# Kernel tuning notes

Measured on AMD Instinct MI355X. Metric: run time of the kernel, lower is better.

Reference implementation:

```python
import jax, jax.numpy as jnp
import numpy as np

P = 3; Q = 3                 # spline degrees (deg_p, deg_q)
OUT_U = 64; OUT_V = 64       # surface evaluation grid
W_CTRL = 1.0; W_SURF = 1.0
B = 1024; MU_MAX = 32; MV_MAX = 32
EPS = 1e-5                   # SurfEval samples u,v in [eps, 1-eps]


def _open_uniform_knots(n_valid, degree, n_max):
    """Clamped open-uniform knot vector for n_valid ctrl pts, padded to static
    length n_max+degree+1. Entries beyond the valid span are clamped to 1.0,
    which makes the padded basis functions identically zero on [eps, 1-eps]."""
    L = n_valid + degree + 1  # true (ragged) knot count, traced int
    k = jnp.arange(n_max + degree + 1)
    interior = k.astype(jnp.float32) / (L - 1).astype(jnp.float32)
    return jnp.where(k <= degree, 0.0, jnp.where(k >= L - 1 - degree, 1.0, interior))


def _bspline_basis(kv, degree, u):
    """Cox-de Boor, vectorized over u. kv: (n_max+degree+1,), u: (U,).
    Returns (U, n_max) basis matrix; padded columns are exactly zero."""
    N = ((u[None, :] >= kv[:-1, None]) & (u[None, :] < kv[1:, None])).astype(jnp.float32)
    for d in range(1, degree + 1):
        m = N.shape[0] - 1  # number of basis funcs at this level
        den1 = kv[d:d + m] - kv[:m]
        den2 = kv[d + 1:d + 1 + m] - kv[1:1 + m]
        s1 = jnp.where((den1 > 0)[:, None],
                       (u[None, :] - kv[:m, None]) / jnp.where(den1 > 0, den1, 1.0)[:, None], 0.0)
        s2 = jnp.where((den2 > 0)[:, None],
                       (kv[d + 1:d + 1 + m, None] - u[None, :]) / jnp.where(den2 > 0, den2, 1.0)[:, None], 0.0)
        N = s1 * N[:m] + s2 * N[1:m + 1]
    return N.T  # (U, n_max)


def _eval_surface(ctrl, mask_b, u, v):
    """NURBS surface eval for one sample with ragged (Mu_i, Mv_i) via padded
    knots/basis; unit weights => rational division by basis partition sum."""
    mu = jnp.maximum(jnp.sum(jnp.any(mask_b > 0, axis=1)), P + 1)
    mv = jnp.maximum(jnp.sum(jnp.any(mask_b > 0, axis=0)), Q + 1)
    Bu = _bspline_basis(_open_uniform_knots(mu, P, MU_MAX), P, u)  # (OUT_U, MU_MAX)
    Bv = _bspline_basis(_open_uniform_knots(mv, Q, MV_MAX), Q, v)  # (OUT_V, MV_MAX)
    num = jnp.einsum('ui,vj,ijd->uvd', Bu, Bv, ctrl)               # (OUT_U, OUT_V, 3)
    den = Bu.sum(-1)[:, None] * Bv.sum(-1)[None, :]                # unit-weight denom
    return num / den[..., None]


def setup_inputs() -> dict:
    key = jax.random.key(0)
    k1, k2, k3, k4, k5 = jax.random.split(key, 5)
    # ragged true control sizes per sample, >= degree+1
    mu = jax.random.randint(k1, (B,), P + 1, MU_MAX + 1)
    mv = jax.random.randint(k2, (B,), Q + 1, MV_MAX + 1)
    mask = ((jnp.arange(MU_MAX)[None, :, None] < mu[:, None, None]) &
            (jnp.arange(MV_MAX)[None, None, :] < mv[:, None, None])).astype(jnp.float32)
    ctrl_pred_pad = jax.random.normal(k3, (B, MU_MAX, MV_MAX, 3), jnp.float32)
    ctrl_gt_pad = jax.random.normal(k4, (B, MU_MAX, MV_MAX, 3), jnp.float32)
    xyz_samples = jax.random.normal(k5, (B, OUT_U, OUT_V, 3), jnp.float32)
    return {"ctrl_pred_pad": ctrl_pred_pad, "ctrl_gt_pad": ctrl_gt_pad,
            "mask": mask, "xyz_samples": xyz_samples}


def reference(ctrl_pred_pad, ctrl_gt_pad, mask, xyz_samples):
    # masked control-point MSE
    diff2 = ((ctrl_pred_pad - ctrl_gt_pad) ** 2).sum(-1)
    loss_ctrl = (diff2 * mask).sum() / jnp.maximum(mask.sum() * 3.0, 1.0)
    # batched ragged surface evaluation
    u = jnp.linspace(EPS, 1.0 - EPS, OUT_U)
    v = jnp.linspace(EPS, 1.0 - EPS, OUT_V)
    surf = jax.vmap(lambda c, m: _eval_surface(c, m, u, v))(ctrl_pred_pad, mask)
    loss_surf = jnp.mean((surf.reshape(B, -1, 3) - xyz_samples.reshape(B, -1, 3)) ** 2)
    total = W_CTRL * loss_ctrl + W_SURF * loss_surf  # original computes total BEFORE nan-guard
    bad = jnp.isnan(surf).any() | jnp.isinf(surf).any()
    surf_mse = jnp.where(bad, jnp.float32(1e6), loss_surf)
    return total, loss_ctrl, surf_mse
```

## Files before the change

### kernel.cpp

```cpp
#include <hip/hip_runtime.h>
#include <math.h>

#define MU_MAXC 32
#define MV_MAXC 32
#define OUT_UC  64
#define OUT_VC  64
#define DEG     3
#define NKNOT   (MU_MAXC + DEG + 1)
#define EPSV    1e-5f

__global__ void zero_ws_kernel(double* acc, int* bad) {
    acc[0] = 0.0; acc[1] = 0.0; acc[2] = 0.0; bad[0] = 0;
}

template <int MODE>
__launch_bounds__(256, 5)
__global__ void nurbs_loss_kernel(const float* __restrict__ ctrl_pred,
                                  const float* __restrict__ ctrl_gt,
                                  const float* __restrict__ mask,
                                  const float* __restrict__ xyz,
                                  double* __restrict__ pd, int Bcnt,
                                  int* __restrict__ badp)
{
    const int b   = blockIdx.x;
    const int tid = threadIdx.x;

    __shared__ float s_tmp[OUT_UC * MV_MAXC * 3];
    __shared__ float s_Bu4[4 * OUT_UC];
    __shared__ float s_Bv4[4 * OUT_VC];
    __shared__ int   s_uoff[OUT_UC];
    __shared__ int   s_voff[OUT_VC];
    __shared__ float s_sumBu[OUT_UC];
    __shared__ float s_sumBv[OUT_VC];
    __shared__ float s_knots_u[NKNOT];
    __shared__ float s_knots_v[NKNOT];
    __shared__ int   s_rowany[MU_MAXC];
    __shared__ int   s_colany[MV_MAXC];
    __shared__ int   s_mu, s_mv, s_bad;
    __shared__ float s_wred[4], s_wred2[4];
    __shared__ float s_ctrl_diff, s_ctrl_mask;

    if (tid < 32) { s_rowany[tid] = 0; s_colany[tid] = 0; }
    if (tid == 0) s_bad = 0;
    __syncthreads();

    float lsum_mask = 0.f, lsum_diff = 0.f;
    for (int k = 0; k < 4; k++) {
        const int cell = tid + 256 * k;
        const int base = (b * 1024 + cell) * 3;
        const float m  = mask[b * 1024 + cell];
        const float p0 = ctrl_pred[base + 0], p1 = ctrl_pred[base + 1], p2 = ctrl_pred[base + 2];
        const float g0 = ctrl_gt[base + 0],   g1 = ctrl_gt[base + 1],   g2 = ctrl_gt[base + 2];
        const float d0 = p0 - g0, d1 = p1 - g1, d2 = p2 - g2;
        lsum_mask += m;
        lsum_diff += m * (d0 * d0 + d1 * d1 + d2 * d2);
        if (m > 0.f) { s_rowany[cell >> 5] = 1; s_colany[cell & 31] = 1; }
    }
    #pragma unroll
    for (int off = 32; off > 0; off >>= 1) {
        lsum_mask += __shfl_down(lsum_mask, off);
        lsum_diff += __shfl_down(lsum_diff, off);
    }
    if ((tid & 63) == 0) { s_wred[tid >> 6] = lsum_mask; s_wred2[tid >> 6] = lsum_diff; }
    __syncthreads();

    if (tid == 0) {
        int cu = 0, cv = 0;
        #pragma unroll
        for (int i = 0; i < 32; i++) { cu += s_rowany[i]; cv += s_colany[i]; }
        s_mu = cu > (DEG + 1) ? cu : (DEG + 1);
        s_mv = cv > (DEG + 1) ? cv : (DEG + 1);
        s_ctrl_mask = s_wred[0] + s_wred[1] + s_wred[2] + s_wred[3];
        s_ctrl_diff = s_wred2[0] + s_wred2[1] + s_wred2[2] + s_wred2[3];
    }
    __syncthreads();

    if (tid < NKNOT) {
        const int L = s_mu + DEG + 1;
        s_knots_u[tid] = (tid <= DEG) ? 0.f
                        : ((tid >= L - 1 - DEG) ? 1.f : (float)tid / (float)(L - 1));
    } else if (tid >= 64 && tid < 64 + NKNOT) {
        const int k = tid - 64;
        const int L = s_mv + DEG + 1;
        s_knots_v[k] = (k <= DEG) ? 0.f
                      : ((k >= L - 1 - DEG) ? 1.f : (float)k / (float)(L - 1));
    }
    __syncthreads();

    if (tid < 128) {
        const bool isU = tid < 64;
        const int t = isU ? tid : (tid - 64);
        const float* kv = isU ? s_knots_u : s_knots_v;
        const float step = (1.f - 2.f * EPSV) / 63.f;
        const float uu = (t == 63) ? (1.f - EPSV) : (EPSV + step * (float)t);

        int span = DEG;
        #pragma unroll
        for (int k = DEG + 1; k < NKNOT - 1; k++)
            if (kv[k] <= uu) span = k;

        float N4[DEG + 1], left[DEG + 1], right[DEG + 1];
        N4[0] = 1.f;
        #pragma unroll
        for (int j = 1; j <= DEG; j++) {
            left[j]  = uu - kv[span + 1 - j];
            right[j] = kv[span + j] - uu;
            float saved = 0.f;
            #pragma unroll
            for (int r = 0; r < j; r++) {
                const float temp = N4[r] / (right[r + 1] + left[j - r]);
                N4[r] = saved + right[r + 1] * temp;
                saved = left[j - r] * temp;
            }
            N4[j] = saved;
        }
        const float s = N4[0] + N4[1] + N4[2] + N4[3];
        const int off = span - DEG;
        if (isU) {
            #pragma unroll
            for (int r = 0; r < 4; r++) s_Bu4[r * 64 + t] = N4[r];
            s_uoff[t] = off; s_sumBu[t] = s;
        } else {
            #pragma unroll
            for (int r = 0; r < 4; r++) s_Bv4[r * 64 + t] = N4[r];
            s_voff[t] = off; s_sumBv[t] = s;
        }
    }
    __syncthreads();

    const float* ctrlb = ctrl_pred + (size_t)b * 1024 * 3;
    for (int k = 0; k < 24; k++) {
        const int flat = tid + 256 * k;
        const int u = flat / 96;
        const int jd = flat - u * 96;
        const int off = s_uoff[u];
        float a = 0.f;
        #pragma unroll
        for (int r = 0; r < 4; r++)
            a += s_Bu4[r * 64 + u] * ctrlb[(off + r) * 96 + jd];
        s_tmp[flat] = a;
    }
    __syncthreads();

    float lsum_surf = 0.f;
    int bad = 0;
    for (int k = 0; k < 16; k++) {
        const int p = tid + 256 * k;
        const int u = p >> 6, v = p & 63;
        const float* tp = &s_tmp[u * 96 + s_voff[v] * 3];
        float n0 = 0.f, n1 = 0.f, n2 = 0.f;
        #pragma unroll
        for (int r = 0; r < 4; r++) {
            const float w = s_Bv4[r * 64 + v];
            n0 += w * tp[r * 3 + 0];
            n1 += w * tp[r * 3 + 1];
            n2 += w * tp[r * 3 + 2];
        }
        const float inv = 1.0f / (s_sumBu[u] * s_sumBv[v]);
        const float x0 = n0 * inv, x1 = n1 * inv, x2 = n2 * inv;
        const int base = (b * 4096 + p) * 3;
        const float d0 = x0 - xyz[base + 0];
        const float d1 = x1 - xyz[base + 1];
        const float d2 = x2 - xyz[base + 2];
        lsum_surf += d0 * d0 + d1 * d1 + d2 * d2;
        if (!isfinite(x0) || !isfinite(x1) || !isfinite(x2)) bad = 1;
    }
    #pragma unroll
    for (int off = 32; off > 0; off >>= 1)
        lsum_surf += __shfl_down(lsum_surf, off);
    if ((tid & 63) == 0) s_wred[tid >> 6] = lsum_surf;
    if (bad) atomicOr(&s_bad, 1);
    __syncthreads();

    if (tid == 0) {
        const double surf = (double)s_wred[0] + s_wred[1] + s_wred[2] + s_wred[3];
        if (MODE == 0) {
            pd[b]             = (double)s_ctrl_diff;
            pd[Bcnt + b]      = (double)s_ctrl_mask;
            pd[2 * Bcnt + b]  = surf;
            badp[b]           = s_bad;
        } else {
            atomicAdd(&pd[0], (double)s_ctrl_diff);
            atomicAdd(&pd[1], (double)s_ctrl_mask);
            atomicAdd(&pd[2], surf);
            if (s_bad) atomicOr(badp, 1);
        }
    }
}

__global__ void finalize_partials_kernel(const double* __restrict__ pd,
                                         const int* __restrict__ badp,
                                         float* __restrict__ out, int Bcnt)
{
    __shared__ double sd0[4], sd1[4], sd2[4];
    __shared__ int sb[4];
    const int tid = threadIdx.x;
    double a0 = 0.0, a1 = 0.0, a2 = 0.0; int bad = 0;
    for (int i = tid; i < Bcnt; i += 256) {
        a0 += pd[i]; a1 += pd[Bcnt + i]; a2 += pd[2 * Bcnt + i];
        bad |= badp[i];
    }
    #pragma unroll
    for (int off = 32; off > 0; off >>= 1) {
        a0 += __shfl_down(a0, off);
        a1 += __shfl_down(a1, off);
        a2 += __shfl_down(a2, off);
        bad |= __shfl_down(bad, off);
    }
    if ((tid & 63) == 0) { const int w = tid >> 6; sd0[w] = a0; sd1[w] = a1; sd2[w] = a2; sb[w] = bad; }
    __syncthreads();
    if (tid == 0) {
        double d0 = 0, d1 = 0, d2 = 0; int bb = 0;
        #pragma unroll
        for (int i = 0; i < 4; i++) { d0 += sd0[i]; d1 += sd1[i]; d2 += sd2[i]; bb |= sb[i]; }
        const double denc = d1 * 3.0;
        const double lc = d0 / (denc > 1.0 ? denc : 1.0);
        const double ls = d2 / ((double)Bcnt * OUT_UC * OUT_VC * 3.0);
        out[0] = (float)(lc + ls);
        out[1] = (float)lc;
        out[2] = bb ? 1.0e6f : (float)ls;
    }
}

__global__ void finalize_atomic_kernel(const double* __restrict__ acc,
                                       const int* __restrict__ bad,
                                       float* __restrict__ out, int Bcnt)
{
    const double denc = acc[1] * 3.0;
    const double lc = acc[0] / (denc > 1.0 ? denc : 1.0);
    const double ls = acc[2] / ((double)Bcnt * OUT_UC * OUT_VC * 3.0);
    out[0] = (float)(lc + ls);
    out[1] = (float)lc;
    out[2] = bad[0] ? 1.0e6f : (float)ls;
}

extern "C" void kernel_launch(void* const* d_in, const int* in_sizes, int n_in,
                              void* d_out, int out_size, void* d_ws, size_t ws_size,
                              hipStream_t stream)
{
    const float* pred = (const float*)d_in[0];
    const float* gt   = (const float*)d_in[1];
    const float* mask = (const float*)d_in[2];
    const float* xyz  = (const float*)d_in[3];
    const int Bcnt = in_sizes[2] / (MU_MAXC * MV_MAXC);

    double* pd = (double*)d_ws;
    float* out = (float*)d_out;

    const size_t need = (size_t)3 * Bcnt * sizeof(double) + (size_t)Bcnt * sizeof(int);
    if (ws_size >= need) {
        int* badp = (int*)(pd + 3 * Bcnt);
        hipLaunchKernelGGL((nurbs_loss_kernel<0>), dim3(Bcnt), dim3(256), 0, stream,
                           pred, gt, mask, xyz, pd, Bcnt, badp);
        hipLaunchKernelGGL(finalize_partials_kernel, dim3(1), dim3(256), 0, stream,
                           pd, badp, out, Bcnt);
    } else {
        int* badp = (int*)(pd + 3);
        hipLaunchKernelGGL(zero_ws_kernel, dim3(1), dim3(1), 0, stream, pd, badp);
        hipLaunchKernelGGL((nurbs_loss_kernel<1>), dim3(Bcnt), dim3(256), 0, stream,
                           pred, gt, mask, xyz, pd, Bcnt, badp);
        hipLaunchKernelGGL(finalize_atomic_kernel, dim3(1), dim3(1), 0, stream,
                           pd, badp, out, Bcnt);
    }
}
```

Before: 115.2 us.

## Fuse finalize into main kernel via last-block atomic counter and vectorize loads

Replaces the partials-plus-finalize two-kernel scheme with one kernel that accumulates into global doubles with atomics, and lets the last block (found via an atomic counter) compute the final outputs. A memset now zeroes the workspace. It also loads the control-point diff with float4 after staging the mask in shared memory, and folds the v-basis normalization into the weights with a precomputed inverse u-sum. The surface loop is restructured so each thread keeps its v weights in registers. This removes one kernel launch and some per-point divisions, in exchange for atomic contention on a few global addresses and a memset call.

```diff
diff --git a/kernel.cpp b/kernel.cpp
--- a/kernel.cpp
+++ b/kernel.cpp
@@ -9,29 +9,26 @@
 #define NKNOT   (MU_MAXC + DEG + 1)
 #define EPSV    1e-5f
 
-__global__ void zero_ws_kernel(double* acc, int* bad) {
-    acc[0] = 0.0; acc[1] = 0.0; acc[2] = 0.0; bad[0] = 0;
-}
-
-template <int MODE>
-__launch_bounds__(256, 5)
-__global__ void nurbs_loss_kernel(const float* __restrict__ ctrl_pred,
-                                  const float* __restrict__ ctrl_gt,
-                                  const float* __restrict__ mask,
-                                  const float* __restrict__ xyz,
-                                  double* __restrict__ pd, int Bcnt,
-                                  int* __restrict__ badp)
+__launch_bounds__(256)
+__global__ void nurbs_loss_fused(const float* __restrict__ ctrl_pred,
+                                 const float* __restrict__ ctrl_gt,
+                                 const float* __restrict__ mask,
+                                 const float* __restrict__ xyz,
+                                 double* __restrict__ acc,
+                                 int* __restrict__ count,
+                                 int* __restrict__ badf,
+                                 float* __restrict__ out, int Bcnt)
 {
     const int b   = blockIdx.x;
     const int tid = threadIdx.x;
 
     __shared__ float s_tmp[OUT_UC * MV_MAXC * 3];
+    __shared__ float s_mask[1024];
     __shared__ float s_Bu4[4 * OUT_UC];
     __shared__ float s_Bv4[4 * OUT_VC];
     __shared__ int   s_uoff[OUT_UC];
     __shared__ int   s_voff[OUT_VC];
-    __shared__ float s_sumBu[OUT_UC];
-    __shared__ float s_sumBv[OUT_VC];
+    __shared__ float s_invSumBu[OUT_UC];
     __shared__ float s_knots_u[NKNOT];
     __shared__ float s_knots_v[NKNOT];
     __shared__ int   s_rowany[MU_MAXC];
@@ -44,17 +41,33 @@
     if (tid == 0) s_bad = 0;
     __syncthreads();
 
-    float lsum_mask = 0.f, lsum_diff = 0.f;
+    float lsum_mask = 0.f;
+    #pragma unroll
     for (int k = 0; k < 4; k++) {
         const int cell = tid + 256 * k;
-        const int base = (b * 1024 + cell) * 3;
         const float m  = mask[b * 1024 + cell];
-        const float p0 = ctrl_pred[base + 0], p1 = ctrl_pred[base + 1], p2 = ctrl_pred[base + 2];
-        const float g0 = ctrl_gt[base + 0],   g1 = ctrl_gt[base + 1],   g2 = ctrl_gt[base + 2];
-        const float d0 = p0 - g0, d1 = p1 - g1, d2 = p2 - g2;
+        s_mask[cell] = m;
         lsum_mask += m;
-        lsum_diff += m * (d0 * d0 + d1 * d1 + d2 * d2);
         if (m > 0.f) { s_rowany[cell >> 5] = 1; s_colany[cell & 31] = 1; }
+    }
+    __syncthreads();
+
+    float lsum_diff = 0.f;
+    {
+        const float4* p4 = (const float4*)(ctrl_pred + (size_t)b * 3072);
+        const float4* g4 = (const float4*)(ctrl_gt   + (size_t)b * 3072);
+        #pragma unroll
+        for (int k = 0; k < 3; k++) {
+            const int e4 = tid + 256 * k;
+            const float4 p = p4[e4];
+            const float4 g = g4[e4];
+            const int e = e4 * 4;
+            const float dx = p.x - g.x, dy = p.y - g.y, dz = p.z - g.z, dw = p.w - g.w;
+            lsum_diff += s_mask[(e + 0) / 3] * dx * dx
+                       + s_mask[(e + 1) / 3] * dy * dy
+                       + s_mask[(e + 2) / 3] * dz * dz
+                       + s_mask[(e + 3) / 3] * dw * dw;
+        }
     }
     #pragma unroll
     for (int off = 32; off > 0; off >>= 1) {
@@ -115,20 +128,21 @@
             N4[j] = saved;
         }
         const float s = N4[0] + N4[1] + N4[2] + N4[3];
+        const float invs = 1.0f / s;
         const int off = span - DEG;
         if (isU) {
             #pragma unroll
             for (int r = 0; r < 4; r++) s_Bu4[r * 64 + t] = N4[r];
-            s_uoff[t] = off; s_sumBu[t] = s;
+            s_uoff[t] = off; s_invSumBu[t] = invs;
         } else {
             #pragma unroll
-            for (int r = 0; r < 4; r++) s_Bv4[r * 64 + t] = N4[r];
-            s_voff[t] = off; s_sumBv[t] = s;
-        }
-    }
-    __syncthreads();
-
-    const float* ctrlb = ctrl_pred + (size_t)b * 1024 * 3;
+            for (int r = 0; r < 4; r++) s_Bv4[r * 64 + t] = N4[r] * invs;
+            s_voff[t] = off;
+        }
+    }
+    __syncthreads();
+
+    const float* ctrlb = ctrl_pred + (size_t)b * 3072;
     for (int k = 0; k < 24; k++) {
         const int flat = tid + 256 * k;
         const int u = flat / 96;
@@ -144,26 +158,29 @@
 
     float lsum_surf = 0.f;
     int bad = 0;
-    for (int k = 0; k < 16; k++) {
-        const int p = tid + 256 * k;
-        const int u = p >> 6, v = p & 63;
-        const float* tp = &s_tmp[u * 96 + s_voff[v] * 3];
-        float n0 = 0.f, n1 = 0.f, n2 = 0.f;
-        #pragma unroll
-        for (int r = 0; r < 4; r++) {
-            const float w = s_Bv4[r * 64 + v];
-            n0 += w * tp[r * 3 + 0];
-            n1 += w * tp[r * 3 + 1];
-            n2 += w * tp[r * 3 + 2];
-        }
-        const float inv = 1.0f / (s_sumBu[u] * s_sumBv[v]);
-        const float x0 = n0 * inv, x1 = n1 * inv, x2 = n2 * inv;
-        const int base = (b * 4096 + p) * 3;
-        const float d0 = x0 - xyz[base + 0];
-        const float d1 = x1 - xyz[base + 1];
-        const float d2 = x2 - xyz[base + 2];
-        lsum_surf += d0 * d0 + d1 * d1 + d2 * d2;
-        if (!isfinite(x0) || !isfinite(x1) || !isfinite(x2)) bad = 1;
+    {
+        const int v = tid & 63;
+        const int voff3 = s_voff[v] * 3;
+        const float w0 = s_Bv4[0 * 64 + v];
+        const float w1 = s_Bv4[1 * 64 + v];
+        const float w2 = s_Bv4[2 * 64 + v];
+        const float w3 = s_Bv4[3 * 64 + v];
+        #pragma unroll
+        for (int k = 0; k < 16; k++) {
+            const int u = (tid >> 6) + 4 * k;
+            const float* tp = &s_tmp[u * 96 + voff3];
+            const float n0 = w0 * tp[0] + w1 * tp[3] + w2 * tp[6] + w3 * tp[9];
+            const float n1 = w0 * tp[1] + w1 * tp[4] + w2 * tp[7] + w3 * tp[10];
+            const float n2 = w0 * tp[2] + w1 * tp[5] + w2 * tp[8] + w3 * tp[11];
+            const float inv = s_invSumBu[u];
+            const float x0 = n0 * inv, x1 = n1 * inv, x2 = n2 * inv;
+            const int base = (b * 4096 + u * 64 + v) * 3;
+            const float d0 = x0 - xyz[base + 0];
+            const float d1 = x1 - xyz[base + 1];
+            const float d2 = x2 - xyz[base + 2];
+            lsum_surf += d0 * d0 + d1 * d1 + d2 * d2;
+            if (!isfinite(x0) || !isfinite(x1) || !isfinite(x2)) bad = 1;
+        }
     }
     #pragma unroll
     for (int off = 32; off > 0; off >>= 1)
@@ -174,64 +191,25 @@
 
     if (tid == 0) {
         const double surf = (double)s_wred[0] + s_wred[1] + s_wred[2] + s_wred[3];
-        if (MODE == 0) {
-            pd[b]             = (double)s_ctrl_diff;
-            pd[Bcnt + b]      = (double)s_ctrl_mask;
-            pd[2 * Bcnt + b]  = surf;
-            badp[b]           = s_bad;
-        } else {
-            atomicAdd(&pd[0], (double)s_ctrl_diff);
-            atomicAdd(&pd[1], (double)s_ctrl_mask);
-            atomicAdd(&pd[2], surf);
-            if (s_bad) atomicOr(badp, 1);
-        }
-    }
-}
-
-__global__ void finalize_partials_kernel(const double* __restrict__ pd,
-                                         const int* __restrict__ badp,
-                                         float* __restrict__ out, int Bcnt)
-{
-    __shared__ double sd0[4], sd1[4], sd2[4];
-    __shared__ int sb[4];
-    const int tid = threadIdx.x;
-    double a0 = 0.0, a1 = 0.0, a2 = 0.0; int bad = 0;
-    for (int i = tid; i < Bcnt; i += 256) {
-        a0 += pd[i]; a1 += pd[Bcnt + i]; a2 += pd[2 * Bcnt + i];
-        bad |= badp[i];
-    }
-    #pragma unroll
-    for (int off = 32; off > 0; off >>= 1) {
-        a0 += __shfl_down(a0, off);
-        a1 += __shfl_down(a1, off);
-        a2 += __shfl_down(a2, off);
-        bad |= __shfl_down(bad, off);
-    }
-    if ((tid & 63) == 0) { const int w = tid >> 6; sd0[w] = a0; sd1[w] = a1; sd2[w] = a2; sb[w] = bad; }
-    __syncthreads();
-    if (tid == 0) {
-        double d0 = 0, d1 = 0, d2 = 0; int bb = 0;
-        #pragma unroll
-        for (int i = 0; i < 4; i++) { d0 += sd0[i]; d1 += sd1[i]; d2 += sd2[i]; bb |= sb[i]; }
-        const double denc = d1 * 3.0;
-        const double lc = d0 / (denc > 1.0 ? denc : 1.0);
-        const double ls = d2 / ((double)Bcnt * OUT_UC * OUT_VC * 3.0);
-        out[0] = (float)(lc + ls);
-        out[1] = (float)lc;
-        out[2] = bb ? 1.0e6f : (float)ls;
-    }
-}
-
-__global__ void finalize_atomic_kernel(const double* __restrict__ acc,
-                                       const int* __restrict__ bad,
-                                       float* __restrict__ out, int Bcnt)
-{
-    const double denc = acc[1] * 3.0;
-    const double lc = acc[0] / (denc > 1.0 ? denc : 1.0);
-    const double ls = acc[2] / ((double)Bcnt * OUT_UC * OUT_VC * 3.0);
-    out[0] = (float)(lc + ls);
-    out[1] = (float)lc;
-    out[2] = bad[0] ? 1.0e6f : (float)ls;
+        atomicAdd(&acc[0], (double)s_ctrl_diff);
+        atomicAdd(&acc[1], (double)s_ctrl_mask);
+        atomicAdd(&acc[2], surf);
+        if (s_bad) atomicOr(badf, 1);
+        __threadfence();
+        const int old = atomicAdd(count, 1);
+        if (old == Bcnt - 1) {
+            const double d0 = atomicAdd(&acc[0], 0.0);
+            const double d1 = atomicAdd(&acc[1], 0.0);
+            const double d2 = atomicAdd(&acc[2], 0.0);
+            const int bb = atomicOr(badf, 0);
+            const double denc = d1 * 3.0;
+            const double lc = d0 / (denc > 1.0 ? denc : 1.0);
+            const double ls = d2 / ((double)Bcnt * OUT_UC * OUT_VC * 3.0);
+            out[0] = (float)(lc + ls);
+            out[1] = (float)lc;
+            out[2] = bb ? 1.0e6f : (float)ls;
+        }
+    }
 }
 
 extern "C" void kernel_launch(void* const* d_in, const int* in_sizes, int n_in,
@@ -244,22 +222,12 @@
     const float* xyz  = (const float*)d_in[3];
     const int Bcnt = in_sizes[2] / (MU_MAXC * MV_MAXC);
 
-    double* pd = (double*)d_ws;
-    float* out = (float*)d_out;
-
-    const size_t need = (size_t)3 * Bcnt * sizeof(double) + (size_t)Bcnt * sizeof(int);
-    if (ws_size >= need) {
-        int* badp = (int*)(pd + 3 * Bcnt);
-        hipLaunchKernelGGL((nurbs_loss_kernel<0>), dim3(Bcnt), dim3(256), 0, stream,
-                           pred, gt, mask, xyz, pd, Bcnt, badp);
-        hipLaunchKernelGGL(finalize_partials_kernel, dim3(1), dim3(256), 0, stream,
-                           pd, badp, out, Bcnt);
-    } else {
-        int* badp = (int*)(pd + 3);
-        hipLaunchKernelGGL(zero_ws_kernel, dim3(1), dim3(1), 0, stream, pd, badp);
-        hipLaunchKernelGGL((nurbs_loss_kernel<1>), dim3(Bcnt), dim3(256), 0, stream,
-                           pred, gt, mask, xyz, pd, Bcnt, badp);
-        hipLaunchKernelGGL(finalize_atomic_kernel, dim3(1), dim3(1), 0, stream,
-                           pd, badp, out, Bcnt);
-    }
+    double* acc = (double*)d_ws;
+    int* count  = (int*)(acc + 3);
+    int* badf   = count + 1;
+    float* out  = (float*)d_out;
+
+    hipMemsetAsync(d_ws, 0, 32, stream);
+    hipLaunchKernelGGL(nurbs_loss_fused, dim3(Bcnt), dim3(256), 0, stream,
+                       pred, gt, mask, xyz, acc, count, badf, out, Bcnt);
 }
```

Measured after the change: 160.3 us. 39.2% more time.
